# Optimization experiments

Hardware: AMD Instinct MI355X
Metric: run time of the kernel (lower is better)

The kernel has to match this reference:

```python
import jax, jax.numpy as jnp
import numpy as np

B, IN, OUT, LMAX = 20000, 128, 128, 6
M = (LMAX + 1) ** 2  # 49

def _make_expand_index(lmax):
    idx = np.zeros((lmax + 1) ** 2, dtype=np.int64)
    for l in range(lmax + 1):
        idx[l * l: l * l + 2 * l + 1] = l
    return jnp.asarray(idx)

def setup_inputs() -> dict:
    key = jax.random.key(0)
    k1, k2 = jax.random.split(key)
    bound = 1.0 / np.sqrt(IN)
    input_embedding = jax.random.normal(k1, (B, M, IN), dtype=jnp.float32)
    weight = jax.random.uniform(k2, (LMAX + 1, OUT, IN), dtype=jnp.float32,
                                minval=-bound, maxval=bound)
    bias = jnp.zeros((OUT,), dtype=jnp.float32)
    expand_index = _make_expand_index(LMAX)
    return {"input_embedding": input_embedding, "weight": weight,
            "bias": bias, "expand_index": expand_index}

def reference(input_embedding, weight, bias, expand_index):
    # gather per-degree weight to per-m weight: [M, out, in]
    w = weight[expand_index]
    # batched per-m matmul: [B, M, in] x [M, out, in] -> [B, M, out]
    out = jnp.einsum('bmi,moi->bmo', input_embedding, w)
    # bias applies only to the l=0 (m=0) row
    out = out.at[:, 0, :].add(bias)
    return out
```

## Files before the change

### kernel.cpp

```cpp
#include <hip/hip_runtime.h>

#define B_TOT   20000
#define M_TOT   49
#define IN_DIM  128
#define OUT_DIM 128
#define TILE_B  128

typedef short v8s __attribute__((ext_vector_type(8)));
typedef float v4f __attribute__((ext_vector_type(4)));

__device__ __forceinline__ short f2bf(float x) {
    union { float f; unsigned int u; } c; c.f = x;
    unsigned int r = c.u + 0x7FFFu + ((c.u >> 16) & 1u);
    return (short)(r >> 16);
}

__global__ __launch_bounds__(256, 3)
void so3_linear_kernel(const float* __restrict__ inp,
                       const float* __restrict__ wgt,
                       const float* __restrict__ bias,
                       float* __restrict__ out) {
    __shared__ __align__(16) short Ws[OUT_DIM][IN_DIM];

    const int tid  = threadIdx.x;
    const int m    = blockIdx.y;
    const int b0   = blockIdx.x * TILE_B;

    int l = 0;
    while ((l + 1) * (l + 1) <= m) ++l;

    const int wave = tid >> 6;
    const int lane = tid & 63;
    const int lr   = lane & 15;
    const int quad = lane >> 4;
    const int wrow = (wave >> 1) * 64;
    const int wcol = (wave & 1) * 64;

    const float* arow[4];
    #pragma unroll
    for (int i = 0; i < 4; ++i) {
        int gb = b0 + wrow + i * 16 + lr;
        int gc = gb < B_TOT ? gb : B_TOT - 1;
        arow[i] = inp + ((size_t)gc * M_TOT + m) * IN_DIM + quad * 8;
    }

    float4 pa[4][2];
    #pragma unroll
    for (int i = 0; i < 4; ++i) {
        pa[i][0] = *(const float4*)(arow[i]);
        pa[i][1] = *(const float4*)(arow[i] + 4);
    }

    const float4* wp4 = (const float4*)(wgt + (size_t)l * OUT_DIM * IN_DIM);
    #pragma unroll
    for (int it = 0; it < 16; ++it) {
        int f  = it * 256 + tid;
        int r  = f >> 5;
        int c4 = f & 31;
        float4 v = wp4[r * (IN_DIM / 4) + c4];
        short4 s;
        s.x = f2bf(v.x); s.y = f2bf(v.y); s.z = f2bf(v.z); s.w = f2bf(v.w);
        int sc = (((c4 >> 1) ^ (r & 15)) << 3) + ((c4 & 1) << 2);
        *(short4*)&Ws[r][sc] = s;
    }

    __syncthreads();

    v4f acc[4][4];
    #pragma unroll
    for (int i = 0; i < 4; ++i)
        #pragma unroll
        for (int j = 0; j < 4; ++j)
            acc[i][j] = (v4f)(0.f);

    #pragma unroll
    for (int kk = 0; kk < 4; ++kk) {
        v8s af[4];
        #pragma unroll
        for (int i = 0; i < 4; ++i) {
            af[i][0] = f2bf(pa[i][0].x); af[i][1] = f2bf(pa[i][0].y);
            af[i][2] = f2bf(pa[i][0].z); af[i][3] = f2bf(pa[i][0].w);
            af[i][4] = f2bf(pa[i][1].x); af[i][5] = f2bf(pa[i][1].y);
            af[i][6] = f2bf(pa[i][1].z); af[i][7] = f2bf(pa[i][1].w);
        }
        if (kk < 3) {
            #pragma unroll
            for (int i = 0; i < 4; ++i) {
                pa[i][0] = *(const float4*)(arow[i] + (kk + 1) * 32);
                pa[i][1] = *(const float4*)(arow[i] + (kk + 1) * 32 + 4);
            }
        }
        const int chunk = kk * 4 + quad;
        const int sc    = ((chunk ^ lr) << 3);
        v8s bf[4];
        #pragma unroll
        for (int j = 0; j < 4; ++j)
            bf[j] = *(const v8s*)&Ws[wcol + j * 16 + lr][sc];
        #pragma unroll
        for (int i = 0; i < 4; ++i)
            #pragma unroll
            for (int j = 0; j < 4; ++j)
                acc[i][j] = __builtin_amdgcn_mfma_f32_16x16x32_bf16(
                                bf[j], af[i], acc[i][j], 0, 0, 0);
    }

    #pragma unroll
    for (int i = 0; i < 4; ++i) {
        const int gb = b0 + wrow + i * 16 + lr;
        if (gb < B_TOT) {
            float* orow = out + ((size_t)gb * M_TOT + m) * OUT_DIM;
            #pragma unroll
            for (int j = 0; j < 4; ++j) {
                const int col = wcol + j * 16 + quad * 4;
                v4f v = acc[i][j];
                if (m == 0) {
                    v[0] += bias[col];
                    v[1] += bias[col + 1];
                    v[2] += bias[col + 2];
                    v[3] += bias[col + 3];
                }
                *(v4f*)(orow + col) = v;
            }
        }
    }
}

extern "C" void kernel_launch(void* const* d_in, const int* in_sizes, int n_in,
                              void* d_out, int out_size, void* d_ws, size_t ws_size,
                              hipStream_t stream) {
    const float* inp  = (const float*)d_in[0];
    const float* wgt  = (const float*)d_in[1];
    const float* bias = (const float*)d_in[2];
    float* out = (float*)d_out;

    dim3 grid((B_TOT + TILE_B - 1) / TILE_B, M_TOT);
    dim3 block(256);
    so3_linear_kernel<<<grid, block, 0, stream>>>(inp, wgt, bias, out);
}
```

Baseline: 884.5 us.

## Stream input tiles via async global-to-LDS DMA with double buffering, weights in registers

The kernel is restructured so each block processes 5 consecutive 32-row batch tiles for one m. Input rows are copied into double-buffered LDS with global_load_lds DMA, and the next tile is prefetched while the current one is computed. Per-degree weights are converted to bf16 once into registers rather than held in LDS. The aim is to overlap the memory-bound input stream with MFMA work and to cut per-block weight setup cost. In exchange it relies on hand-written vmcnt waits, carries higher register pressure, and drops the batch bounds checks, which is valid only because 20000 divides evenly into 160-row blocks.

```diff
diff --git a/kernel.cpp b/kernel.cpp
--- a/kernel.cpp
+++ b/kernel.cpp
@@ -4,10 +4,12 @@
 #define M_TOT   49
 #define IN_DIM  128
 #define OUT_DIM 128
-#define TILE_B  128
+#define TILE_B  32
+#define NT      5
+#define BX      125
 
-typedef short v8s __attribute__((ext_vector_type(8)));
-typedef float v4f __attribute__((ext_vector_type(4)));
+typedef short  v8s __attribute__((ext_vector_type(8)));
+typedef float  v4f __attribute__((ext_vector_type(4)));
 
 __device__ __forceinline__ short f2bf(float x) {
     union { float f; unsigned int u; } c; c.f = x;
@@ -15,112 +17,124 @@
     return (short)(r >> 16);
 }
 
-__global__ __launch_bounds__(256, 3)
+typedef __attribute__((address_space(1))) void* gas_ptr;
+typedef __attribute__((address_space(3))) void* las_ptr;
+
+__device__ __forceinline__ void dma16(const void* g, void* s) {
+    __builtin_amdgcn_global_load_lds((gas_ptr)g, (las_ptr)s, 16, 0, 0);
+}
+
+__global__ __launch_bounds__(256, 4)
 void so3_linear_kernel(const float* __restrict__ inp,
                        const float* __restrict__ wgt,
                        const float* __restrict__ bias,
                        float* __restrict__ out) {
-    __shared__ __align__(16) short Ws[OUT_DIM][IN_DIM];
+    __shared__ __align__(16) float As[2][TILE_B][IN_DIM];
 
-    const int tid  = threadIdx.x;
-    const int m    = blockIdx.y;
-    const int b0   = blockIdx.x * TILE_B;
-
+    const int tid = threadIdx.x;
+    const int m   = blockIdx.y;
     int l = 0;
     while ((l + 1) * (l + 1) <= m) ++l;
 
-    const int wave = tid >> 6;
     const int lane = tid & 63;
     const int lr   = lane & 15;
     const int quad = lane >> 4;
-    const int wrow = (wave >> 1) * 64;
-    const int wcol = (wave & 1) * 64;
+    const int wave = tid >> 6;
+    const int wr   = wave & 1;
+    const int wc   = wave >> 1;
 
-    const float* arow[4];
+    const int b_blk0 = blockIdx.x * (NT * TILE_B);
+
     #pragma unroll
-    for (int i = 0; i < 4; ++i) {
-        int gb = b0 + wrow + i * 16 + lr;
-        int gc = gb < B_TOT ? gb : B_TOT - 1;
-        arow[i] = inp + ((size_t)gc * M_TOT + m) * IN_DIM + quad * 8;
+    for (int it = 0; it < 4; ++it) {
+        int C  = it * 256 + tid;
+        int r  = C >> 5;
+        int cs = C & 31;
+        int c  = cs ^ (r & 7);
+        const float* src = inp + ((size_t)(b_blk0 + r) * M_TOT + m) * IN_DIM + c * 4;
+        dma16(src, &As[0][0][0] + C * 4);
     }
 
-    float4 pa[4][2];
-    #pragma unroll
-    for (int i = 0; i < 4; ++i) {
-        pa[i][0] = *(const float4*)(arow[i]);
-        pa[i][1] = *(const float4*)(arow[i] + 4);
+    v8s bw[4][4];
+    {
+        const float* wb = wgt + (size_t)l * OUT_DIM * IN_DIM
+                        + (size_t)(wc * 64 + lr) * IN_DIM + quad * 8;
+        #pragma unroll
+        for (int j = 0; j < 4; ++j) {
+            #pragma unroll
+            for (int kk = 0; kk < 4; ++kk) {
+                const float* p = wb + j * 16 * IN_DIM + kk * 32;
+                float4 w0 = *(const float4*)(p);
+                float4 w1 = *(const float4*)(p + 4);
+                v8s f;
+                f[0] = f2bf(w0.x); f[1] = f2bf(w0.y);
+                f[2] = f2bf(w0.z); f[3] = f2bf(w0.w);
+                f[4] = f2bf(w1.x); f[5] = f2bf(w1.y);
+                f[6] = f2bf(w1.z); f[7] = f2bf(w1.w);
+                bw[kk][j] = f;
+            }
+        }
     }
 
-    const float4* wp4 = (const float4*)(wgt + (size_t)l * OUT_DIM * IN_DIM);
-    #pragma unroll
-    for (int it = 0; it < 16; ++it) {
-        int f  = it * 256 + tid;
-        int r  = f >> 5;
-        int c4 = f & 31;
-        float4 v = wp4[r * (IN_DIM / 4) + c4];
-        short4 s;
-        s.x = f2bf(v.x); s.y = f2bf(v.y); s.z = f2bf(v.z); s.w = f2bf(v.w);
-        int sc = (((c4 >> 1) ^ (r & 15)) << 3) + ((c4 & 1) << 2);
-        *(short4*)&Ws[r][sc] = s;
-    }
-
-    __syncthreads();
-
-    v4f acc[4][4];
-    #pragma unroll
-    for (int i = 0; i < 4; ++i)
-        #pragma unroll
-        for (int j = 0; j < 4; ++j)
-            acc[i][j] = (v4f)(0.f);
+    const int arow = wr * 16 + lr;
+    const int sw   = arow & 7;
 
     #pragma unroll
-    for (int kk = 0; kk < 4; ++kk) {
-        v8s af[4];
-        #pragma unroll
-        for (int i = 0; i < 4; ++i) {
-            af[i][0] = f2bf(pa[i][0].x); af[i][1] = f2bf(pa[i][0].y);
-            af[i][2] = f2bf(pa[i][0].z); af[i][3] = f2bf(pa[i][0].w);
-            af[i][4] = f2bf(pa[i][1].x); af[i][5] = f2bf(pa[i][1].y);
-            af[i][6] = f2bf(pa[i][1].z); af[i][7] = f2bf(pa[i][1].w);
-        }
-        if (kk < 3) {
+    for (int t = 0; t < NT; ++t) {
+        const int cur = t & 1;
+
+        if (t + 1 < NT) {
+            const int tb = b_blk0 + (t + 1) * TILE_B;
             #pragma unroll
-            for (int i = 0; i < 4; ++i) {
-                pa[i][0] = *(const float4*)(arow[i] + (kk + 1) * 32);
-                pa[i][1] = *(const float4*)(arow[i] + (kk + 1) * 32 + 4);
+            for (int it = 0; it < 4; ++it) {
+                int C  = it * 256 + tid;
+                int r  = C >> 5;
+                int cs = C & 31;
+                int c  = cs ^ (r & 7);
+                const float* src = inp + ((size_t)(tb + r) * M_TOT + m) * IN_DIM + c * 4;
+                dma16(src, &As[cur ^ 1][0][0] + C * 4);
             }
         }
-        const int chunk = kk * 4 + quad;
-        const int sc    = ((chunk ^ lr) << 3);
-        v8s bf[4];
+
+        if (t == 0 || t == NT - 1)
+            asm volatile("s_waitcnt vmcnt(4)" ::: "memory");
+        else
+            asm volatile("s_waitcnt vmcnt(8)" ::: "memory");
+        asm volatile("s_barrier" ::: "memory");
+
+        v4f acc[4];
         #pragma unroll
-        for (int j = 0; j < 4; ++j)
-            bf[j] = *(const v8s*)&Ws[wcol + j * 16 + lr][sc];
+        for (int j = 0; j < 4; ++j) acc[j] = (v4f)(0.f);
+
         #pragma unroll
-        for (int i = 0; i < 4; ++i)
+        for (int kk = 0; kk < 4; ++kk) {
+            const int c0 = (kk * 8 + quad * 2)     ^ sw;
+            const int c1 = (kk * 8 + quad * 2 + 1) ^ sw;
+            v4f a0 = *(const v4f*)&As[cur][arow][c0 * 4];
+            v4f a1 = *(const v4f*)&As[cur][arow][c1 * 4];
+            v8s af;
+            af[0] = f2bf(a0[0]); af[1] = f2bf(a0[1]);
+            af[2] = f2bf(a0[2]); af[3] = f2bf(a0[3]);
+            af[4] = f2bf(a1[0]); af[5] = f2bf(a1[1]);
+            af[6] = f2bf(a1[2]); af[7] = f2bf(a1[3]);
             #pragma unroll
             for (int j = 0; j < 4; ++j)
-                acc[i][j] = __builtin_amdgcn_mfma_f32_16x16x32_bf16(
-                                bf[j], af[i], acc[i][j], 0, 0, 0);
-    }
+                acc[j] = __builtin_amdgcn_mfma_f32_16x16x32_bf16(
+                             bw[kk][j], af, acc[j], 0, 0, 0);
+        }
 
-    #pragma unroll
-    for (int i = 0; i < 4; ++i) {
-        const int gb = b0 + wrow + i * 16 + lr;
-        if (gb < B_TOT) {
-            float* orow = out + ((size_t)gb * M_TOT + m) * OUT_DIM;
-            #pragma unroll
-            for (int j = 0; j < 4; ++j) {
-                const int col = wcol + j * 16 + quad * 4;
-                v4f v = acc[i][j];
-                if (m == 0) {
-                    v[0] += bias[col];
-                    v[1] += bias[col + 1];
-                    v[2] += bias[col + 2];
-                    v[3] += bias[col + 3];
-                }
-                *(v4f*)(orow + col) = v;
+        asm volatile("s_barrier" ::: "memory");
+
+        const int gb = b_blk0 + t * TILE_B + wr * 16 + lr;
+        float* orow = out + ((size_t)gb * M_TOT + m) * OUT_DIM + wc * 64 + quad * 4;
+        #pragma unroll
+        for (int j = 0; j < 4; ++j) {
+            v4f v = acc[j];
+            if (m == 0) {
+                const v4f bv = *(const v4f*)&bias[wc * 64 + j * 16 + quad * 4];
+                v += bv;
             }
+            *(v4f*)(orow + j * 16) = v;
         }
     }
 }
@@ -133,7 +147,7 @@
     const float* bias = (const float*)d_in[2];
     float* out = (float*)d_out;
 
-    dim3 grid((B_TOT + TILE_B - 1) / TILE_B, M_TOT);
+    dim3 grid(BX, M_TOT);
     dim3 block(256);
     so3_linear_kernel<<<grid, block, 0, stream>>>(inp, wgt, bias, out);
 }
```

After: 928.8 us. 1.05x slower.
